# Optimization experiments

Measured on AMD Instinct MI355X. Metric: run time of the kernel, lower is better.

Reference implementation:

```python
import jax, jax.numpy as jnp
import numpy as np

NUM_STEPS = 128
STEP = 1.0 / (NUM_STEPS - 1)
N, D = 262144, 128


def setup_inputs() -> dict:
    key = jax.random.key(0)
    k0, k1, k2 = jax.random.split(key, 3)
    return {
        "feat_t0": jax.random.normal(k0, (N, D), dtype=jnp.float32),
        "feat_t1": jax.random.normal(k1, (N, D), dtype=jnp.float32),
        "label": jax.random.randint(k2, (N,), 0, 2),
    }


def _histogram(s, idx, inds, size):
    # s: [N] similarities in [0,1]; idx: [N] = floor(s/step) bin index (constant wrt grad)
    # t_j = j*STEP, j in [0, NUM_STEPS). Matches the torch masked-assign logic:
    #   indsa: delta == t - step  ->  w = (s - t + step)/step
    #   indsb: delta == t         ->  w = (-s + t + step)/step
    #   else 0; masked by class indicator `inds`; sum over samples / size.
    j = jnp.arange(NUM_STEPS, dtype=jnp.int32)[:, None]      # [T,1]
    t = j.astype(s.dtype) * STEP                              # [T,1]
    indsa = (idx[None, :] == (j - 1)) & inds[None, :]         # [T,N]
    indsb = (idx[None, :] == j) & inds[None, :]               # [T,N]
    wa = (s[None, :] - t + STEP) / STEP                       # [T,N]
    wb = (-s[None, :] + t + STEP) / STEP                      # [T,N]
    w = jnp.where(indsa, wa, 0.0) + jnp.where(indsb, wb, 0.0)
    return w.sum(axis=1) / size                               # [T]


def reference(feat_t0, feat_t1, label):
    # cosine similarity between the two temporal feature maps, mapped to [0,1]
    n0 = feat_t0 / jnp.linalg.norm(feat_t0, axis=1, keepdims=True)
    n1 = feat_t1 / jnp.linalg.norm(feat_t1, axis=1, keepdims=True)
    sim = jnp.sum(n0 * n1, axis=1)                            # [N] in [-1,1]
    s = jnp.clip((sim + 1.0) * 0.5, 0.0, 1.0)                 # [N] in [0,1]
    idx = jnp.floor(s / STEP).astype(jnp.int32)               # bin index (delta = idx*step)

    pos = label == 1  # changed pixels
    neg = label == 0  # unchanged pixels
    pos_size = jnp.maximum(pos.sum(), 1).astype(s.dtype)
    neg_size = jnp.maximum(neg.sum(), 1).astype(s.dtype)

    hist_pos = _histogram(s, idx, pos, pos_size)              # [T]
    hist_neg = _histogram(s, idx, neg, neg_size)              # [T]

    # histogram loss: probability that a negative similarity exceeds a positive one
    loss = jnp.sum(jnp.cumsum(hist_pos) * hist_neg)
    return loss
```

## Files before the change

kernel.cpp:

```cpp
#include <hip/hip_runtime.h>

#define T 128
#define STEPF (1.0f/127.0f)
#define NCOPY 8
#define WSSTRIDE 258


__global__ __launch_bounds__(256) void sim_hist_kernel(
    const float* __restrict__ A, const float* __restrict__ B,
    const int* __restrict__ label, float* __restrict__ ws, int n) {
  __shared__ float hloc[2 * T];
  __shared__ unsigned int ccnt;
  const int tid = threadIdx.x;
  hloc[tid] = 0.0f;
  if (tid == 0) ccnt = 0u;
  __syncthreads();

  const int lane4 = tid & 3;
  const int row   = (blockIdx.x * 256 + tid) >> 2;
  int cnt = 0;

  if (row < n) {
    const float4* __restrict__ a = (const float4*)A + (size_t)row * 32 + lane4;
    const float4* __restrict__ b = (const float4*)B + (size_t)row * 32 + lane4;
    float ab = 0.f, aa = 0.f, bb = 0.f;
#pragma unroll
    for (int k = 0; k < 8; ++k) {
      const float4 va = a[k * 4];
      const float4 vb = b[k * 4];
      ab = fmaf(va.x, vb.x, fmaf(va.y, vb.y, fmaf(va.z, vb.z, fmaf(va.w, vb.w, ab))));
      aa = fmaf(va.x, va.x, fmaf(va.y, va.y, fmaf(va.z, va.z, fmaf(va.w, va.w, aa))));
      bb = fmaf(vb.x, vb.x, fmaf(vb.y, vb.y, fmaf(vb.z, vb.z, fmaf(vb.w, vb.w, bb))));
    }
    ab += __shfl_xor(ab, 1); ab += __shfl_xor(ab, 2);
    aa += __shfl_xor(aa, 1); aa += __shfl_xor(aa, 2);
    bb += __shfl_xor(bb, 1); bb += __shfl_xor(bb, 2);

    if (lane4 == 0) {
      const int lab = (label[row] == 1) ? 1 : 0;
      cnt = lab;
      const float sim = ab * rsqrtf(aa * bb);
      float s = fminf(fmaxf((sim + 1.0f) * 0.5f, 0.0f), 1.0f);
      const float idxf = floorf(s / STEPF);
      const int idx = (int)idxf;
      const float w0 = (-s + idxf * STEPF + STEPF) / STEPF;
      atomicAdd(&hloc[lab * T + idx], w0);
      if (idx + 1 < T) {
        const float w1 = (s - (idxf + 1.0f) * STEPF + STEPF) / STEPF;
        atomicAdd(&hloc[lab * T + idx + 1], w1);
      }
    }
  }

#pragma unroll
  for (int off = 32; off > 0; off >>= 1) cnt += __shfl_xor(cnt, off);
  if ((tid & 63) == 0 && cnt) atomicAdd(&ccnt, (unsigned int)cnt);
  __syncthreads();

  float* wsc = ws + (blockIdx.x & (NCOPY - 1)) * WSSTRIDE;
  const float v = hloc[tid];
  if (v != 0.0f) atomicAdd(&wsc[tid], v);
  if (tid == 0 && ccnt) atomicAdd((unsigned int*)(wsc + 2 * T), ccnt);
}

__global__ void finalize_kernel(const float* __restrict__ ws, float* __restrict__ out, int n) {
  const int lane = threadIdx.x & 63;
  unsigned int cpos = 0;
  float hp0 = 0.f, hp1 = 0.f, hn0 = 0.f, hn1 = 0.f;
  const int j0 = 2 * lane, j1 = 2 * lane + 1;
#pragma unroll
  for (int c = 0; c < NCOPY; ++c) {
    const float* wsc = ws + c * WSSTRIDE;
    hn0 += wsc[j0];       hn1 += wsc[j1];
    hp0 += wsc[T + j0];   hp1 += wsc[T + j1];
    cpos += ((const unsigned int*)(wsc + 2 * T))[0];
  }
  const float possz = fmaxf((float)cpos, 1.0f);
  const float negsz = fmaxf((float)(n - (int)cpos), 1.0f);
  hp0 /= possz; hp1 /= possz;
  hn0 /= negsz; hn1 /= negsz;

  const float pair = hp0 + hp1;
  float scan = pair;
#pragma unroll
  for (int off = 1; off < 64; off <<= 1) {
    const float u = __shfl_up(scan, off);
    if (lane >= off) scan += u;
  }
  const float excl = scan - pair;
  float part = (excl + hp0) * hn0 + (excl + hp0 + hp1) * hn1;
#pragma unroll
  for (int off = 32; off > 0; off >>= 1) part += __shfl_xor(part, off);
  if (lane == 0) out[0] = part;
}

extern "C" void kernel_launch(void* const* d_in, const int* in_sizes, int n_in,
                              void* d_out, int out_size, void* d_ws, size_t ws_size,
                              hipStream_t stream) {
  const float* A  = (const float*)d_in[0];
  const float* B  = (const float*)d_in[1];
  const int* lab  = (const int*)d_in[2];
  const int n = in_sizes[2];
  float* ws = (float*)d_ws;

  hipMemsetAsync(d_ws, 0, NCOPY * WSSTRIDE * sizeof(float), stream);

  const int grid = (n + 63) / 64;
  sim_hist_kernel<<<grid, 256, 0, stream>>>(A, B, lab, ws, n);
  finalize_kernel<<<1, 64, 0, stream>>>(ws, (float*)d_out, n);
}
```

Measured before the change: 55.70 us.

## Stage feature rows into LDS via direct global-to-LDS loads with XOR swizzle

After: 52.46 us. 5.8% less time.

```diff
diff --git a/kernel.cpp b/kernel.cpp
--- a/kernel.cpp
+++ b/kernel.cpp
@@ -1,4 +1,5 @@
 #include <hip/hip_runtime.h>
+#include <stdint.h>
 
 #define T 128
 #define STEPF (1.0f/127.0f)
@@ -6,9 +7,14 @@
 #define WSSTRIDE 258
 
 
+#define GLOAD(gp, lp) __builtin_amdgcn_global_load_lds(                        \
+    (const __attribute__((address_space(1))) void*)(gp),                       \
+    (__attribute__((address_space(3))) void*)(lp), 16, 0, 0)
+
 __global__ __launch_bounds__(256) void sim_hist_kernel(
     const float* __restrict__ A, const float* __restrict__ B,
     const int* __restrict__ label, float* __restrict__ ws, int n) {
+  __shared__ __align__(16) float tile[16384];
   __shared__ float hloc[2 * T];
   __shared__ unsigned int ccnt;
   const int tid = threadIdx.x;
@@ -16,45 +22,68 @@
   if (tid == 0) ccnt = 0u;
   __syncthreads();
 
-  const int lane4 = tid & 3;
-  const int row   = (blockIdx.x * 256 + tid) >> 2;
+  const int w      = tid >> 6;
+  const int lam    = tid & 63;
+  const int lhalf  = lam >> 5;
+  const int c32    = lam & 31;
+  const int g      = tid >> 2;
+  const int gl     = g & 15;
+  const int l      = tid & 3;
+  const size_t rowbase = (size_t)blockIdx.x * 64 + w * 16;
+
+  const int lv = label[blockIdx.x * 64 + g];
+
+#pragma unroll
+  for (int i = 0; i < 8; ++i) {
+    const int r  = 2 * i + lhalf;
+    const int cg = c32 ^ ((r & 7) << 2);
+    GLOAD(A + (rowbase + r) * 128 + cg * 4, &tile[w * 4096 + i * 256]);
+  }
+#pragma unroll
+  for (int i = 0; i < 8; ++i) {
+    const int r  = 2 * i + lhalf;
+    const int cg = c32 ^ ((r & 7) << 2);
+    GLOAD(B + (rowbase + r) * 128 + cg * 4, &tile[w * 4096 + 2048 + i * 256]);
+  }
+  asm volatile("s_waitcnt vmcnt(0)" ::: "memory");
+  __builtin_amdgcn_sched_barrier(0);
+
+  const float* At = &tile[w * 4096 + gl * 128];
+  const float* Bt = &tile[w * 4096 + 2048 + gl * 128];
+  const int sw = (gl & 7) << 2;
+  float ab = 0.f, aa = 0.f, bb = 0.f;
+#pragma unroll
+  for (int k = 0; k < 8; ++k) {
+    const int c = (l + 4 * k) ^ sw;
+    const float4 va = *(const float4*)&At[c * 4];
+    const float4 vb = *(const float4*)&Bt[c * 4];
+    ab = fmaf(va.x, vb.x, fmaf(va.y, vb.y, fmaf(va.z, vb.z, fmaf(va.w, vb.w, ab))));
+    aa = fmaf(va.x, va.x, fmaf(va.y, va.y, fmaf(va.z, va.z, fmaf(va.w, va.w, aa))));
+    bb = fmaf(vb.x, vb.x, fmaf(vb.y, vb.y, fmaf(vb.z, vb.z, fmaf(vb.w, vb.w, bb))));
+  }
+  ab += __shfl_xor(ab, 1); ab += __shfl_xor(ab, 2);
+  aa += __shfl_xor(aa, 1); aa += __shfl_xor(aa, 2);
+  bb += __shfl_xor(bb, 1); bb += __shfl_xor(bb, 2);
+
   int cnt = 0;
-
-  if (row < n) {
-    const float4* __restrict__ a = (const float4*)A + (size_t)row * 32 + lane4;
-    const float4* __restrict__ b = (const float4*)B + (size_t)row * 32 + lane4;
-    float ab = 0.f, aa = 0.f, bb = 0.f;
-#pragma unroll
-    for (int k = 0; k < 8; ++k) {
-      const float4 va = a[k * 4];
-      const float4 vb = b[k * 4];
-      ab = fmaf(va.x, vb.x, fmaf(va.y, vb.y, fmaf(va.z, vb.z, fmaf(va.w, vb.w, ab))));
-      aa = fmaf(va.x, va.x, fmaf(va.y, va.y, fmaf(va.z, va.z, fmaf(va.w, va.w, aa))));
-      bb = fmaf(vb.x, vb.x, fmaf(vb.y, vb.y, fmaf(vb.z, vb.z, fmaf(vb.w, vb.w, bb))));
-    }
-    ab += __shfl_xor(ab, 1); ab += __shfl_xor(ab, 2);
-    aa += __shfl_xor(aa, 1); aa += __shfl_xor(aa, 2);
-    bb += __shfl_xor(bb, 1); bb += __shfl_xor(bb, 2);
-
-    if (lane4 == 0) {
-      const int lab = (label[row] == 1) ? 1 : 0;
-      cnt = lab;
-      const float sim = ab * rsqrtf(aa * bb);
-      float s = fminf(fmaxf((sim + 1.0f) * 0.5f, 0.0f), 1.0f);
-      const float idxf = floorf(s / STEPF);
-      const int idx = (int)idxf;
-      const float w0 = (-s + idxf * STEPF + STEPF) / STEPF;
-      atomicAdd(&hloc[lab * T + idx], w0);
-      if (idx + 1 < T) {
-        const float w1 = (s - (idxf + 1.0f) * STEPF + STEPF) / STEPF;
-        atomicAdd(&hloc[lab * T + idx + 1], w1);
-      }
+  if (l == 0) {
+    const int lab = (lv == 1) ? 1 : 0;
+    cnt = lab;
+    const float sim = ab * rsqrtf(aa * bb);
+    float s = fminf(fmaxf((sim + 1.0f) * 0.5f, 0.0f), 1.0f);
+    const float idxf = floorf(s / STEPF);
+    const int idx = (int)idxf;
+    const float w0 = (-s + idxf * STEPF + STEPF) / STEPF;
+    atomicAdd(&hloc[lab * T + idx], w0);
+    if (idx + 1 < T) {
+      const float w1 = (s - (idxf + 1.0f) * STEPF + STEPF) / STEPF;
+      atomicAdd(&hloc[lab * T + idx + 1], w1);
     }
   }
 
 #pragma unroll
   for (int off = 32; off > 0; off >>= 1) cnt += __shfl_xor(cnt, off);
-  if ((tid & 63) == 0 && cnt) atomicAdd(&ccnt, (unsigned int)cnt);
+  if (lam == 0 && cnt) atomicAdd(&ccnt, (unsigned int)cnt);
   __syncthreads();
 
   float* wsc = ws + (blockIdx.x & (NCOPY - 1)) * WSSTRIDE;
@@ -105,7 +134,7 @@
 
   hipMemsetAsync(d_ws, 0, NCOPY * WSSTRIDE * sizeof(float), stream);
 
-  const int grid = (n + 63) / 64;
+  const int grid = n >> 6;
   sim_hist_kernel<<<grid, 256, 0, stream>>>(A, B, lab, ws, n);
   finalize_kernel<<<1, 64, 0, stream>>>(ws, (float*)d_out, n);
 }
```
